# Optimization experiments

Measured on AMD Instinct MI355X. Metric: run time of the kernel, lower is better.

The kernel has to match this reference:

```python
import jax, jax.numpy as jnp
import numpy as np

N_QUBITS = 10
N_LAYERS = 4
BATCH = 16384
IN_FEAT = 256
HIDDEN = 128


def _ry(theta):
    # RY(theta) = [[cos(t/2), -sin(t/2)], [sin(t/2), cos(t/2)]]; theta: (B, n) -> (B, n, 2, 2)
    c = jnp.cos(theta / 2)
    s = jnp.sin(theta / 2)
    row0 = jnp.stack([c, -s], axis=-1)
    row1 = jnp.stack([s, c], axis=-1)
    return jnp.stack([row0, row1], axis=-2).astype(jnp.complex64)


def _rot(phi, theta, omega):
    # PennyLane Rot = RZ(omega) RY(theta) RZ(phi)
    c = jnp.cos(theta / 2)
    s = jnp.sin(theta / 2)
    ep = jnp.exp(-0.5j * (phi + omega))  # e^{-i(phi+omega)/2}
    em = jnp.exp(-0.5j * (phi - omega))  # e^{-i(phi-omega)/2}
    m00 = ep * c
    m01 = -jnp.conj(em) * s
    m10 = em * s
    m11 = jnp.conj(ep) * c
    return jnp.stack([jnp.stack([m00, m01]), jnp.stack([m10, m11])]).astype(jnp.complex64)


def _apply_1q(state, gate, w, n):
    # state: (B, 2**n); gate: (2,2) shared or (B,2,2) per-sample; wire w (wire 0 = MSB)
    B = state.shape[0]
    L, R = 2 ** w, 2 ** (n - w - 1)
    s = state.reshape(B, L, 2, R)
    if gate.ndim == 3:
        s = jnp.einsum('xab,xlbr->xlar', gate, s)
    else:
        s = jnp.einsum('ab,xlbr->xlar', gate, s)
    return s.reshape(B, -1)


def _cnot_perm(n, c, t):
    # CNOT is a basis permutation: flip target bit where control bit is 1 (static numpy)
    idx = np.arange(2 ** n)
    flip = idx ^ (1 << (n - 1 - t))
    ctrl = (idx >> (n - 1 - c)) & 1
    return np.where(ctrl == 1, flip, idx)


def _z_signs(n):
    # (n, 2**n) of +/-1: sign of PauliZ on each wire for each basis state
    idx = np.arange(2 ** n)
    bits = (idx[None, :] >> (n - 1 - np.arange(n)[:, None])) & 1
    return (1.0 - 2.0 * bits).astype(np.float32)


def _circuit(angles, qw):
    # angles: (B, n) embedding angles; qw: (L, n, 3) StronglyEntanglingLayers weights
    B, n = angles.shape
    L = qw.shape[0]
    state = jnp.zeros((B, 2 ** n), jnp.complex64).at[:, 0].set(1.0)
    ry = _ry(angles)  # (B, n, 2, 2) per-sample AngleEmbedding RY gates
    for w in range(n):
        state = _apply_1q(state, ry[:, w], w, n)
    for l in range(L):
        for w in range(n):
            state = _apply_1q(state, _rot(qw[l, w, 0], qw[l, w, 1], qw[l, w, 2]), w, n)
        r = (l % (n - 1)) + 1  # default StronglyEntanglingLayers ranges
        for i in range(n):
            state = state[:, _cnot_perm(n, i, (i + r) % n)]
    probs = jnp.abs(state) ** 2  # (B, 2**n)
    return probs @ jnp.asarray(_z_signs(n)).T  # (B, n) expval PauliZ per wire


def setup_inputs() -> dict:
    key = jax.random.key(0)
    ks = jax.random.split(key, 10)
    d = {
        'x': jax.random.normal(ks[0], (BATCH, IN_FEAT), jnp.float32),
        'W1': jax.random.normal(ks[1], (HIDDEN, IN_FEAT), jnp.float32) / np.sqrt(IN_FEAT),
        'b1': jnp.zeros((HIDDEN,), jnp.float32),
        'W2': jax.random.normal(ks[2], (N_QUBITS, HIDDEN), jnp.float32) / np.sqrt(HIDDEN),
        'b2': jnp.zeros((N_QUBITS,), jnp.float32),
        'q_weights': jax.random.normal(ks[3], (N_LAYERS, N_QUBITS, 3), jnp.float32) * 0.1,
        'W3': jax.random.normal(ks[4], (HIDDEN, N_QUBITS), jnp.float32) / np.sqrt(N_QUBITS),
        'b3': jnp.zeros((HIDDEN,), jnp.float32),
        'W4': jax.random.normal(ks[5], (1, HIDDEN), jnp.float32) / np.sqrt(HIDDEN),
        'b4': jnp.zeros((1,), jnp.float32),
    }
    return d


def reference(x, W1, b1, W2, b2, q_weights, W3, b3, W4, b4):
    # Encoder (dropout is identity in eval mode)
    h = jax.nn.relu(x @ W1.T + b1)
    angles = jnp.tanh(h @ W2.T + b2)  # (B, n_qubits)
    # Batched quantum state-vector simulation
    q = _circuit(angles, q_weights).astype(jnp.float32)  # (B, n_qubits)
    # Decoder
    d = jax.nn.relu(q @ W3.T + b3)
    return d @ W4.T + b4  # (B, 1)
```

## Files before the change

kernel.cpp:

```cpp
#include <hip/hip_runtime.h>
#include <math.h>

#define BATCH 16384
#define INFEAT 256
#define HID 128
#define NQ 10
#define NL 4
#define GSTRIDE 48

typedef float v2f __attribute__((ext_vector_type(2)));

template<int M>
__device__ __forceinline__ float lxor(float x) {
    if constexpr (M == 0) {
        return x;
    } else if constexpr (M < 4) {
        constexpr int ctrl = (0 ^ M) | ((1 ^ M) << 2) | ((2 ^ M) << 4) | ((3 ^ M) << 6);
        return __int_as_float(__builtin_amdgcn_update_dpp(
            __float_as_int(x), __float_as_int(x), ctrl, 0xF, 0xF, false));
    } else if constexpr (M == 8) {
        return __int_as_float(__builtin_amdgcn_update_dpp(
            __float_as_int(x), __float_as_int(x), 0x128, 0xF, 0xF, false));
    } else if constexpr (M < 32) {
        return __int_as_float(__builtin_amdgcn_ds_swizzle(
            __float_as_int(x), (M << 10) | 0x1F));
    } else {
        return __shfl_xor(x, M, 64);
    }
}

__device__ __forceinline__ float dpp_sum(float v) {
    v += __int_as_float(__builtin_amdgcn_update_dpp(0, __float_as_int(v), 0x111, 0xF, 0xF, true));
    v += __int_as_float(__builtin_amdgcn_update_dpp(0, __float_as_int(v), 0x112, 0xF, 0xF, true));
    v += __int_as_float(__builtin_amdgcn_update_dpp(0, __float_as_int(v), 0x114, 0xF, 0xF, true));
    v += __int_as_float(__builtin_amdgcn_update_dpp(0, __float_as_int(v), 0x118, 0xF, 0xF, true));
    v += __int_as_float(__builtin_amdgcn_update_dpp(0, __float_as_int(v), 0x142, 0xF, 0xF, true));
    v += __int_as_float(__builtin_amdgcn_update_dpp(0, __float_as_int(v), 0x143, 0xF, 0xF, true));
    return __int_as_float(__builtin_amdgcn_readlane(__float_as_int(v), 63));
}

template<int HALF>
__device__ __forceinline__ void swap_pl(float& a, float& b) {
    if constexpr (HALF == 32)
        asm("v_permlane32_swap_b32 %0, %1" : "+v"(a), "+v"(b));
    else
        asm("v_permlane16_swap_b32 %0, %1" : "+v"(a), "+v"(b));
}

__device__ __forceinline__ v2f pks_mul(v2f c, v2f a) {
    v2f d; asm("v_pk_mul_f32 %0, %1, %2" : "=v"(d) : "s"(c), "v"(a)); return d;
}
__device__ __forceinline__ v2f pks_fma(v2f c, v2f a, v2f b) {
    v2f d; asm("v_pk_fma_f32 %0, %1, %2, %3" : "=v"(d) : "s"(c), "v"(a), "v"(b)); return d;
}
__device__ __forceinline__ v2f pkv_mul_c(v2f c, v2f a) {
    v2f d; asm("v_pk_mul_f32 %0, %1, %2 op_sel:[0,0] op_sel_hi:[0,1]"
               : "=v"(d) : "v"(c), "v"(a)); return d;
}
__device__ __forceinline__ v2f pkv_fma_c(v2f c, v2f a, v2f b) {
    v2f d; asm("v_pk_fma_f32 %0, %1, %2, %3 op_sel:[0,0,0] op_sel_hi:[0,1,1]"
               : "=v"(d) : "v"(c), "v"(a), "v"(b)); return d;
}
__device__ __forceinline__ v2f pks_mul_blo(v2f c, v2f a) {
    v2f d; asm("v_pk_mul_f32 %0, %1, %2 op_sel:[0,0] op_sel_hi:[1,0]"
               : "=v"(d) : "s"(c), "v"(a)); return d;
}
__device__ __forceinline__ v2f pks_fma_blo(v2f c, v2f a, v2f b) {
    v2f d; asm("v_pk_fma_f32 %0, %1, %2, %3 op_sel:[0,0,0] op_sel_hi:[1,0,1]"
               : "=v"(d) : "s"(c), "v"(a), "v"(b)); return d;
}
__device__ __forceinline__ v2f pks_fma_bhi(v2f c, v2f a, v2f b) {
    v2f d; asm("v_pk_fma_f32 %0, %1, %2, %3 op_sel:[0,1,0] op_sel_hi:[1,1,1]"
               : "=v"(d) : "s"(c), "v"(a), "v"(b)); return d;
}

__device__ __forceinline__ float getv(const v2f (&A)[8], int e) {
    return (e & 1) ? A[e >> 1].y : A[e >> 1].x;
}
__device__ __forceinline__ void setv(v2f (&A)[8], int e, float v) {
    if (e & 1) A[e >> 1].y = v; else A[e >> 1].x = v;
}

template<int KM>
__device__ __forceinline__ void reg_gate_asm(const float* __restrict__ g,
                                             v2f (&AR)[8], v2f (&AI)[8]) {
    const v2f* __restrict__ gp = (const v2f*)g;
    const v2f c00r = gp[6],  c00i = gp[7],  c00in = gp[8];
    const v2f c01r = gp[9],  c01i = gp[10], c01in = gp[11];
    const v2f c10r = gp[12], c10i = gp[13], c10in = gp[14];
    const v2f c11r = gp[15], c11i = gp[16], c11in = gp[17];
#pragma unroll
    for (int k0 = 0; k0 < 8; ++k0) {
        if (k0 & KM) continue;
        const int k1 = k0 | KM;
        v2f A0 = AR[k0], I0 = AI[k0], A1 = AR[k1], I1 = AI[k1];
        v2f t = pks_mul(c00r, A0); t = pks_fma(c00in, I0, t);
        t = pks_fma(c01r, A1, t);  AR[k0] = pks_fma(c01in, I1, t);
        v2f u = pks_mul(c00r, I0); u = pks_fma(c00i, A0, u);
        u = pks_fma(c01r, I1, u);  AI[k0] = pks_fma(c01i, A1, u);
        v2f t2 = pks_mul(c10r, A0); t2 = pks_fma(c10in, I0, t2);
        t2 = pks_fma(c11r, A1, t2); AR[k1] = pks_fma(c11in, I1, t2);
        v2f u2 = pks_mul(c10r, I0); u2 = pks_fma(c10i, A0, u2);
        u2 = pks_fma(c11r, I1, u2); AI[k1] = pks_fma(c11i, A1, u2);
    }
}

__device__ __forceinline__ void reg_gate_q3_asm(const float* __restrict__ g,
                                                v2f (&AR)[8], v2f (&AI)[8]) {
    const v2f* __restrict__ gp = (const v2f*)g;
    const v2f P0 = gp[18], P1 = gp[19], P1n = gp[20];
    const v2f P2 = gp[21], P3 = gp[22], P3n = gp[23];
#pragma unroll
    for (int k = 0; k < 8; ++k) {
        v2f t = pks_mul_blo(P0, AR[k]);
        t = pks_fma_blo(P1n, AI[k], t);
        t = pks_fma_bhi(P2, AR[k], t);
        v2f nR = pks_fma_bhi(P3n, AI[k], t);
        v2f u = pks_mul_blo(P0, AI[k]);
        u = pks_fma_blo(P1, AR[k], u);
        u = pks_fma_bhi(P2, AI[k], u);
        v2f nI = pks_fma_bhi(P3, AR[k], u);
        AR[k] = nR; AI[k] = nI;
    }
}

template<int LB>
__device__ __forceinline__ void lane_gate_asm(const float* __restrict__ g, int lane,
                                              v2f (&AR)[8], v2f (&AI)[8]) {
    const bool side = (lane >> LB) & 1;
    v2f Cmr, Cmi, Cmin, Cpr, Cpi, Cpin;
    Cmr.x  = side ? g[6]  : g[0];
    Cmi.x  = side ? g[7]  : g[1];
    Cmin.x = side ? g[11] : g[8];
    Cpr.x  = side ? g[4]  : g[2];
    Cpi.x  = side ? g[5]  : g[3];
    Cpin.x = side ? g[10] : g[9];
#pragma unroll
    for (int k = 0; k < 8; ++k) {
        v2f PR, PI;
        PR.x = lxor<(1 << LB)>(AR[k].x); PR.y = lxor<(1 << LB)>(AR[k].y);
        PI.x = lxor<(1 << LB)>(AI[k].x); PI.y = lxor<(1 << LB)>(AI[k].y);
        v2f t = pkv_mul_c(Cmr, AR[k]); t = pkv_fma_c(Cmin, AI[k], t);
        t = pkv_fma_c(Cpr, PR, t);     v2f NR = pkv_fma_c(Cpin, PI, t);
        v2f u = pkv_mul_c(Cmr, AI[k]); u = pkv_fma_c(Cmi, AR[k], u);
        u = pkv_fma_c(Cpr, PI, u);     v2f NI = pkv_fma_c(Cpi, PR, u);
        AR[k] = NR; AI[k] = NI;
    }
}

template<int HALF>
__device__ __forceinline__ void lane_gate_pl_asm(const float* __restrict__ g,
                                                 v2f (&AR)[8], v2f (&AI)[8]) {
    const v2f* __restrict__ gp = (const v2f*)g;
    const v2f c00r = gp[6],  c00i = gp[7],  c00in = gp[8];
    const v2f c01r = gp[9],  c01i = gp[10], c01in = gp[11];
    const v2f c10r = gp[12], c10i = gp[13], c10in = gp[14];
    const v2f c11r = gp[15], c11i = gp[16], c11in = gp[17];
#pragma unroll
    for (int k0 = 0; k0 < 8; k0 += 2) {
        const int k1 = k0 + 1;
        float Xr0 = AR[k0].x, Xr1 = AR[k0].y, Yr0 = AR[k1].x, Yr1 = AR[k1].y;
        float Xi0 = AI[k0].x, Xi1 = AI[k0].y, Yi0 = AI[k1].x, Yi1 = AI[k1].y;
        swap_pl<HALF>(Xr0, Yr0); swap_pl<HALF>(Xr1, Yr1);
        swap_pl<HALF>(Xi0, Yi0); swap_pl<HALF>(Xi1, Yi1);
        v2f Xr; Xr.x = Xr0; Xr.y = Xr1;  v2f Yr; Yr.x = Yr0; Yr.y = Yr1;
        v2f Xi; Xi.x = Xi0; Xi.y = Xi1;  v2f Yi; Yi.x = Yi0; Yi.y = Yi1;
        v2f t = pks_mul(c00r, Xr); t = pks_fma(c00in, Xi, t);
        t = pks_fma(c01r, Yr, t);  v2f Pr = pks_fma(c01in, Yi, t);
        v2f u = pks_mul(c00r, Xi); u = pks_fma(c00i, Xr, u);
        u = pks_fma(c01r, Yi, u);  v2f Pi = pks_fma(c01i, Yr, u);
        v2f t2 = pks_mul(c10r, Xr); t2 = pks_fma(c10in, Xi, t2);
        t2 = pks_fma(c11r, Yr, t2); v2f Qr = pks_fma(c11in, Yi, t2);
        v2f u2 = pks_mul(c10r, Xi); u2 = pks_fma(c10i, Xr, u2);
        u2 = pks_fma(c11r, Yi, u2); v2f Qi = pks_fma(c11i, Yr, u2);
        float pr0 = Pr.x, pr1 = Pr.y, qr0 = Qr.x, qr1 = Qr.y;
        float pi0 = Pi.x, pi1 = Pi.y, qi0 = Qi.x, qi1 = Qi.y;
        swap_pl<HALF>(pr0, qr0); swap_pl<HALF>(pr1, qr1);
        swap_pl<HALF>(pi0, qi0); swap_pl<HALF>(pi1, qi1);
        AR[k0].x = pr0; AR[k0].y = pr1; AR[k1].x = qr0; AR[k1].y = qr1;
        AI[k0].x = pi0; AI[k0].y = pi1; AI[k1].x = qi0; AI[k1].y = qi1;
    }
}

constexpr int rr_src(int rs, int e) {
    int s = e;
    for (int i = 3 - rs; i >= 0; --i) s ^= ((s >> (3 - i)) & 1) << (3 - i - rs);
    return s;
}
constexpr int rl_mask(int rs, int e) {
    int m = 0;
    for (int i = (4 - rs < 0 ? 0 : 4 - rs); i <= 3; ++i)
        if ((e >> (3 - i)) & 1) m |= 1 << (9 - i - rs);
    return m;
}

template<int L>
__device__ __forceinline__ void do_gates(const float* __restrict__ gt, int lane,
                                         v2f (&AR)[8], v2f (&AI)[8]) {
    const float* __restrict__ gb = gt + L * NQ * GSTRIDE;
    reg_gate_asm<4>(gb + 0 * GSTRIDE, AR, AI);
    reg_gate_asm<2>(gb + 1 * GSTRIDE, AR, AI);
    reg_gate_asm<1>(gb + 2 * GSTRIDE, AR, AI);
    reg_gate_q3_asm(gb + 3 * GSTRIDE, AR, AI);
    lane_gate_pl_asm<32>(gb + 4 * GSTRIDE, AR, AI);
    lane_gate_pl_asm<16>(gb + 5 * GSTRIDE, AR, AI);
    lane_gate_asm<3>(gb + 6 * GSTRIDE, lane, AR, AI);
    lane_gate_asm<2>(gb + 7 * GSTRIDE, lane, AR, AI);
    lane_gate_asm<1>(gb + 8 * GSTRIDE, lane, AR, AI);
    lane_gate_asm<0>(gb + 9 * GSTRIDE, lane, AR, AI);
}

template<int L>
__device__ __forceinline__ void do_move(int lane, v2f (&AR)[8], v2f (&AI)[8]) {
    constexpr int rs = L + 1;
    int y = lane;
#pragma unroll
    for (int i = 9 - rs; i >= 4; --i)
        y ^= ((y >> (9 - i)) & 1) << (9 - i - rs);
    const int base = y << 2;
    {
        float nr[16], ni[16];
#pragma unroll
        for (int e = 0; e < 16; ++e) {
            const int src = rr_src(rs, e);
            const int am  = rl_mask(rs, e) << 2;
            nr[e] = __int_as_float(__builtin_amdgcn_ds_bpermute(base ^ am, __float_as_int(getv(AR, src))));
            ni[e] = __int_as_float(__builtin_amdgcn_ds_bpermute(base ^ am, __float_as_int(getv(AI, src))));
        }
#pragma unroll
        for (int k = 0; k < 8; ++k) {
            AR[k].x = nr[2 * k]; AR[k].y = nr[2 * k + 1];
            AI[k].x = ni[2 * k]; AI[k].y = ni[2 * k + 1];
        }
    }
#pragma unroll
    for (int i = 10 - rs; i <= 9; ++i) {
        const bool p = (lane >> (9 - i)) & 1;
        const int tm = 1 << (13 - i - rs);
#pragma unroll
        for (int e = 0; e < 16; ++e) {
            if (!(e & tm)) {
                const int e1 = e | tm;
                float v0r = getv(AR, e), v1r = getv(AR, e1);
                setv(AR, e, p ? v1r : v0r); setv(AR, e1, p ? v0r : v1r);
                float v0i = getv(AI, e), v1i = getv(AI, e1);
                setv(AI, e, p ? v1i : v0i); setv(AI, e1, p ? v0i : v1i);
            }
        }
    }
}

__device__ __forceinline__ float ftanh(float s) {
    float e = __expf(2.f * s);
    return 1.f - 2.f / (e + 1.f);
}

__global__ void prep_kernel(const float* __restrict__ qw, const float* __restrict__ W1,
                            float* __restrict__ gtab, float* __restrict__ w1q) {
    int tid = blockIdx.x * 256 + threadIdx.x;
    if (tid < 128 * 64) {
        int k2 = tid >> 6, l = tid & 63;
        float4 q;
        q.x = W1[(size_t)(2 * l)     * INFEAT + 2 * k2];
        q.y = W1[(size_t)(2 * l + 1) * INFEAT + 2 * k2];
        q.z = W1[(size_t)(2 * l)     * INFEAT + 2 * k2 + 1];
        q.w = W1[(size_t)(2 * l + 1) * INFEAT + 2 * k2 + 1];
        ((float4*)w1q)[tid] = q;
    }
    if (blockIdx.x == 0 && threadIdx.x < NL * NQ) {
        int t = threadIdx.x;
        float phi = qw[t * 3 + 0], th = qw[t * 3 + 1], om = qw[t * 3 + 2];
        float c = __cosf(th * 0.5f), s = __sinf(th * 0.5f);
        float a = 0.5f * (phi + om), b = 0.5f * (phi - om);
        float ca = __cosf(a), sa = __sinf(a);
        float cb = __cosf(b), sb = __sinf(b);
        float m00r = ca * c,  m00i = -sa * c;
        float m01r = -cb * s, m01i = -sb * s;
        float m10r = cb * s,  m10i = -sb * s;
        float m11r = ca * c,  m11i = sa * c;
        float* g = gtab + t * GSTRIDE;
        g[0] = m00r; g[1] = m00i; g[2] = m01r; g[3] = m01i;
        g[4] = m10r; g[5] = m10i; g[6] = m11r; g[7] = m11i;
        g[8] = -m00i; g[9] = -m01i; g[10] = -m10i; g[11] = -m11i;
        g[12] = g[13] = m00r;  g[14] = g[15] = m00i;  g[16] = g[17] = -m00i;
        g[18] = g[19] = m01r;  g[20] = g[21] = m01i;  g[22] = g[23] = -m01i;
        g[24] = g[25] = m10r;  g[26] = g[27] = m10i;  g[28] = g[29] = -m10i;
        g[30] = g[31] = m11r;  g[32] = g[33] = m11i;  g[34] = g[35] = -m11i;
        g[36] = m00r;  g[37] = m10r;
        g[38] = m00i;  g[39] = m10i;
        g[40] = -m00i; g[41] = -m10i;
        g[42] = m01r;  g[43] = m11r;
        g[44] = m01i;  g[45] = m11i;
        g[46] = -m01i; g[47] = -m11i;
    }
}

__global__ __launch_bounds__(256, 4) void fused_kernel(
    const float* __restrict__ x, const float* __restrict__ w1q,
    const float* __restrict__ b1, const float* __restrict__ W2,
    const float* __restrict__ b2, const float* __restrict__ gtab,
    const float* __restrict__ W3, const float* __restrict__ b3,
    const float* __restrict__ W4, const float* __restrict__ b4,
    float* __restrict__ out)
{
    __shared__ float w3s[HID * 11];
    __shared__ float b3s[HID], w4s[HID];
    __shared__ float b4s;
    __shared__ v2f hpart[4][4][64];

    const int t = threadIdx.x;
    for (int f = t; f < HID * NQ; f += 256) {
        int c = f / NQ, k = f - c * NQ;
        w3s[c * 11 + k] = W3[f];
    }
    if (t < HID) { b3s[t] = b3[t]; w4s[t] = W4[t]; }
    if (t == 0) b4s = b4[0];

    const int lane = t & 63;
    const int wid = t >> 6;
    const int row0 = blockIdx.x * 4;
    const int ukw = __builtin_amdgcn_readfirstlane(wid);

    v2f acc[4];
#pragma unroll
    for (int r = 0; r < 4; ++r) acc[r] = (v2f)(0.f);
    const float4* __restrict__ xr0 = (const float4*)(x + (size_t)(row0 + 0) * INFEAT + ukw * 64);
    const float4* __restrict__ xr1 = (const float4*)(x + (size_t)(row0 + 1) * INFEAT + ukw * 64);
    const float4* __restrict__ xr2 = (const float4*)(x + (size_t)(row0 + 2) * INFEAT + ukw * 64);
    const float4* __restrict__ xr3 = (const float4*)(x + (size_t)(row0 + 3) * INFEAT + ukw * 64);
    const float4* __restrict__ w1p = (const float4*)w1q + (size_t)ukw * 32 * 64 + lane;
#pragma unroll 4
    for (int kk4 = 0; kk4 < 16; ++kk4) {
        float4 x0 = xr0[kk4], x1 = xr1[kk4], x2 = xr2[kk4], x3 = xr3[kk4];
        float xk[4][4] = {{x0.x, x0.y, x0.z, x0.w}, {x1.x, x1.y, x1.z, x1.w},
                          {x2.x, x2.y, x2.z, x2.w}, {x3.x, x3.y, x3.z, x3.w}};
        float4 q0 = w1p[(2 * kk4 + 0) * 64];
        float4 q1 = w1p[(2 * kk4 + 1) * 64];
        v2f w0; w0.x = q0.x; w0.y = q0.y;
        v2f w1; w1.x = q0.z; w1.y = q0.w;
        v2f w2; w2.x = q1.x; w2.y = q1.y;
        v2f w3; w3.x = q1.z; w3.y = q1.w;
#pragma unroll
        for (int r = 0; r < 4; ++r) {
            v2f xb;
            xb.x = xk[r][0]; xb.y = xk[r][0];
            acc[r] = __builtin_elementwise_fma(xb, w0, acc[r]);
            xb.x = xk[r][1]; xb.y = xk[r][1];
            acc[r] = __builtin_elementwise_fma(xb, w1, acc[r]);
            xb.x = xk[r][2]; xb.y = xk[r][2];
            acc[r] = __builtin_elementwise_fma(xb, w2, acc[r]);
            xb.x = xk[r][3]; xb.y = xk[r][3];
            acc[r] = __builtin_elementwise_fma(xb, w3, acc[r]);
        }
    }
#pragma unroll
    for (int r = 0; r < 4; ++r) hpart[wid][r][lane] = acc[r];
    __syncthreads();

    v2f hs = hpart[0][wid][lane];
    hs += hpart[1][wid][lane];
    hs += hpart[2][wid][lane];
    hs += hpart[3][wid][lane];
    float2 b1v = ((const float2*)b1)[lane];
    float h0 = fmaxf(hs.x + b1v.x, 0.f);
    float h1 = fmaxf(hs.y + b1v.y, 0.f);

    const int row = row0 + wid;

    float cth[NQ], sth[NQ];
#pragma unroll
    for (int w = 0; w < NQ; ++w) {
        float2 w2v = ((const float2*)(W2 + (size_t)w * HID))[lane];
        float aw = dpp_sum(fmaf(h0, w2v.x, h1 * w2v.y)) + b2[w];
        float th = ftanh(aw) * 0.5f;
        cth[w] = __cosf(th); sth[w] = __sinf(th);
    }

    float Lr, Li;
    {
        const float* __restrict__ g = gtab + 4 * GSTRIDE;
        bool bw = (lane >> 5) & 1;
        float g0 = bw ? g[4] : g[0], g1 = bw ? g[5] : g[1];
        float g2 = bw ? g[6] : g[2], g3 = bw ? g[7] : g[3];
        Lr = fmaf(g0, cth[4], g2 * sth[4]);
        Li = fmaf(g1, cth[4], g3 * sth[4]);
    }
#pragma unroll
    for (int w = 5; w < 10; ++w) {
        const float* __restrict__ g = gtab + w * GSTRIDE;
        bool bw = (lane >> (9 - w)) & 1;
        float g0 = bw ? g[4] : g[0], g1 = bw ? g[5] : g[1];
        float g2 = bw ? g[6] : g[2], g3 = bw ? g[7] : g[3];
        float fr = fmaf(g0, cth[w], g2 * sth[w]);
        float fi = fmaf(g1, cth[w], g3 * sth[w]);
        float nr = Lr * fr - Li * fi;
        float ni = Lr * fi + Li * fr;
        Lr = nr; Li = ni;
    }
    float q01r[4], q01i[4], q23r[4], q23i[4];
    {
        const float* __restrict__ ga = gtab + 0 * GSTRIDE;
        const float* __restrict__ gb = gtab + 1 * GSTRIDE;
        float a0r = fmaf(ga[0], cth[0], ga[2] * sth[0]);
        float a0i = fmaf(ga[1], cth[0], ga[3] * sth[0]);
        float b0r = fmaf(ga[4], cth[0], ga[6] * sth[0]);
        float b0i = fmaf(ga[5], cth[0], ga[7] * sth[0]);
        float a1r = fmaf(gb[0], cth[1], gb[2] * sth[1]);
        float a1i = fmaf(gb[1], cth[1], gb[3] * sth[1]);
        float b1r = fmaf(gb[4], cth[1], gb[6] * sth[1]);
        float b1i = fmaf(gb[5], cth[1], gb[7] * sth[1]);
#pragma unroll
        for (int j = 0; j < 4; ++j) {
            float f0r = (j & 2) ? b0r : a0r, f0i = (j & 2) ? b0i : a0i;
            float f1r = (j & 1) ? b1r : a1r, f1i = (j & 1) ? b1i : a1i;
            q01r[j] = f0r * f1r - f0i * f1i;
            q01i[j] = f0r * f1i + f0i * f1r;
        }
    }
    {
        const float* __restrict__ ga = gtab + 2 * GSTRIDE;
        const float* __restrict__ gb = gtab + 3 * GSTRIDE;
        float a2r = fmaf(ga[0], cth[2], ga[2] * sth[2]);
        float a2i = fmaf(ga[1], cth[2], ga[3] * sth[2]);
        float b2r = fmaf(ga[4], cth[2], ga[6] * sth[2]);
        float b2i = fmaf(ga[5], cth[2], ga[7] * sth[2]);
        float a3r = fmaf(gb[0], cth[3], gb[2] * sth[3]);
        float a3i = fmaf(gb[1], cth[3], gb[3] * sth[3]);
        float b3r = fmaf(gb[4], cth[3], gb[6] * sth[3]);
        float b3i = fmaf(gb[5], cth[3], gb[7] * sth[3]);
#pragma unroll
        for (int j = 0; j < 4; ++j) {
            float f2r = (j & 2) ? b2r : a2r, f2i = (j & 2) ? b2i : a2i;
            float f3r = (j & 1) ? b3r : a3r, f3i = (j & 1) ? b3i : a3i;
            q23r[j] = f2r * f3r - f2i * f3i;
            q23i[j] = f2r * f3i + f2i * f3r;
        }
    }
    v2f AR[8], AI[8];
#pragma unroll
    for (int e = 0; e < 16; ++e) {
        const int jh = e >> 2, jl = e & 3;
        float tr = q01r[jh] * q23r[jl] - q01i[jh] * q23i[jl];
        float ti = q01r[jh] * q23i[jl] + q01i[jh] * q23r[jl];
        float ar = tr * Lr - ti * Li;
        float ai = tr * Li + ti * Lr;
        setv(AR, e, ar); setv(AI, e, ai);
    }

    do_move<0>(lane, AR, AI);
    do_gates<1>(gtab, lane, AR, AI);
    do_move<1>(lane, AR, AI);
    do_gates<2>(gtab, lane, AR, AI);
    do_move<2>(lane, AR, AI);
    do_gates<3>(gtab, lane, AR, AI);
    do_move<3>(lane, AR, AI);

    v2f Pk[8];
#pragma unroll
    for (int k = 0; k < 8; ++k) Pk[k] = AR[k] * AR[k] + AI[k] * AI[k];
    v2f S = Pk[0] + Pk[1] + Pk[2] + Pk[3] + Pk[4] + Pk[5] + Pk[6] + Pk[7];
    float ptot = S.x + S.y;
    v2f Sq0 = Pk[4] + Pk[5] + Pk[6] + Pk[7];
    v2f Sq1 = Pk[2] + Pk[3] + Pk[6] + Pk[7];
    v2f Sq2 = Pk[1] + Pk[3] + Pk[5] + Pk[7];
    float es0 = dpp_sum(ptot - 2.f * (Sq0.x + Sq0.y));
    float es1 = dpp_sum(ptot - 2.f * (Sq1.x + Sq1.y));
    float es2 = dpp_sum(ptot - 2.f * (Sq2.x + Sq2.y));
    float es3 = dpp_sum(ptot - 2.f * S.y);
    float Wv = ptot;
    {
        float p;
        p = lxor<1>(Wv);  Wv = (lane & 1)  ? p - Wv : Wv + p;
        p = lxor<2>(Wv);  Wv = (lane & 2)  ? p - Wv : Wv + p;
        p = lxor<4>(Wv);  Wv = (lane & 4)  ? p - Wv : Wv + p;
        p = lxor<8>(Wv);  Wv = (lane & 8)  ? p - Wv : Wv + p;
        p = lxor<16>(Wv); Wv = (lane & 16) ? p - Wv : Wv + p;
        p = lxor<32>(Wv); Wv = (lane & 32) ? p - Wv : Wv + p;
    }
    const int wvi = __float_as_int(Wv);
    float es[NQ];
    es[0] = es0; es[1] = es1; es[2] = es2; es[3] = es3;
    es[4] = __int_as_float(__builtin_amdgcn_readlane(wvi, 32));
    es[5] = __int_as_float(__builtin_amdgcn_readlane(wvi, 16));
    es[6] = __int_as_float(__builtin_amdgcn_readlane(wvi, 8));
    es[7] = __int_as_float(__builtin_amdgcn_readlane(wvi, 4));
    es[8] = __int_as_float(__builtin_amdgcn_readlane(wvi, 2));
    es[9] = __int_as_float(__builtin_amdgcn_readlane(wvi, 1));

    float accv = 0.f;
#pragma unroll
    for (int j = 0; j < 2; ++j) {
        int c = lane + 64 * j;
        float d = b3s[c];
#pragma unroll
        for (int k = 0; k < NQ; ++k) d = fmaf(w3s[c * 11 + k], es[k], d);
        d = fmaxf(d, 0.f);
        accv = fmaf(d, w4s[c], accv);
    }
    accv = dpp_sum(accv);
    if (lane == 0) out[row] = accv + b4s;
}

extern "C" void kernel_launch(void* const* d_in, const int* in_sizes, int n_in,
                              void* d_out, int out_size, void* d_ws, size_t ws_size,
                              hipStream_t stream) {
    const float* x  = (const float*)d_in[0];
    const float* W1 = (const float*)d_in[1];
    const float* b1 = (const float*)d_in[2];
    const float* W2 = (const float*)d_in[3];
    const float* b2 = (const float*)d_in[4];
    const float* qw = (const float*)d_in[5];
    const float* W3 = (const float*)d_in[6];
    const float* b3 = (const float*)d_in[7];
    const float* W4 = (const float*)d_in[8];
    const float* b4 = (const float*)d_in[9];
    float* gtab = (float*)d_ws;
    float* w1q  = (float*)d_ws + 2048;
    float* out  = (float*)d_out;

    prep_kernel<<<(128 * 64 + 255) / 256, 256, 0, stream>>>(qw, W1, gtab, w1q);
    fused_kernel<<<BATCH / 4, 256, 0, stream>>>(x, w1q, b1, W2, b2, gtab, W3, b3, W4, b4, out);
}
```

Measured before the change: 214.9 us.

## Factor Rot gates into real RY plus merged diagonal phase tables

Each PennyLane Rot gate is split as RZ·RY·RZ. All RZ phases between consecutive RY layers, including those carried through the CNOT permutation, are folded into one precomputed per-basis-state diagonal phase table. The 10 general complex gates per layer become real RY rotations with far fewer packed FMAs, plus one complex diagonal multiply per layer loaded from a workspace table. The cost is extra global or L2 loads of the phase table (8 float4 per lane per layer) and a heavier prep kernel computing the phases in double precision.

```diff
diff --git a/kernel.cpp b/kernel.cpp
--- a/kernel.cpp
+++ b/kernel.cpp
@@ -53,6 +53,10 @@
 __device__ __forceinline__ v2f pks_fma(v2f c, v2f a, v2f b) {
     v2f d; asm("v_pk_fma_f32 %0, %1, %2, %3" : "=v"(d) : "s"(c), "v"(a), "v"(b)); return d;
 }
+__device__ __forceinline__ v2f pks_fma_swap(v2f c, v2f a, v2f b) {
+    v2f d; asm("v_pk_fma_f32 %0, %1, %2, %3 op_sel:[0,1,0] op_sel_hi:[1,0,1]"
+               : "=v"(d) : "s"(c), "v"(a), "v"(b)); return d;
+}
 __device__ __forceinline__ v2f pkv_mul_c(v2f c, v2f a) {
     v2f d; asm("v_pk_mul_f32 %0, %1, %2 op_sel:[0,0] op_sel_hi:[0,1]"
                : "=v"(d) : "v"(c), "v"(a)); return d;
@@ -61,18 +65,6 @@
     v2f d; asm("v_pk_fma_f32 %0, %1, %2, %3 op_sel:[0,0,0] op_sel_hi:[0,1,1]"
                : "=v"(d) : "v"(c), "v"(a), "v"(b)); return d;
 }
-__device__ __forceinline__ v2f pks_mul_blo(v2f c, v2f a) {
-    v2f d; asm("v_pk_mul_f32 %0, %1, %2 op_sel:[0,0] op_sel_hi:[1,0]"
-               : "=v"(d) : "s"(c), "v"(a)); return d;
-}
-__device__ __forceinline__ v2f pks_fma_blo(v2f c, v2f a, v2f b) {
-    v2f d; asm("v_pk_fma_f32 %0, %1, %2, %3 op_sel:[0,0,0] op_sel_hi:[1,0,1]"
-               : "=v"(d) : "s"(c), "v"(a), "v"(b)); return d;
-}
-__device__ __forceinline__ v2f pks_fma_bhi(v2f c, v2f a, v2f b) {
-    v2f d; asm("v_pk_fma_f32 %0, %1, %2, %3 op_sel:[0,1,0] op_sel_hi:[1,1,1]"
-               : "=v"(d) : "s"(c), "v"(a), "v"(b)); return d;
-}
 
 __device__ __forceinline__ float getv(const v2f (&A)[8], int e) {
     return (e & 1) ? A[e >> 1].y : A[e >> 1].x;
@@ -81,81 +73,40 @@
     if (e & 1) A[e >> 1].y = v; else A[e >> 1].x = v;
 }
 
+
 template<int KM>
-__device__ __forceinline__ void reg_gate_asm(const float* __restrict__ g,
-                                             v2f (&AR)[8], v2f (&AI)[8]) {
+__device__ __forceinline__ void reg_ry(const float* __restrict__ g,
+                                       v2f (&AR)[8], v2f (&AI)[8]) {
     const v2f* __restrict__ gp = (const v2f*)g;
-    const v2f c00r = gp[6],  c00i = gp[7],  c00in = gp[8];
-    const v2f c01r = gp[9],  c01i = gp[10], c01in = gp[11];
-    const v2f c10r = gp[12], c10i = gp[13], c10in = gp[14];
-    const v2f c11r = gp[15], c11i = gp[16], c11in = gp[17];
+    const v2f C = gp[6], S = gp[7], Sn = gp[8];
 #pragma unroll
     for (int k0 = 0; k0 < 8; ++k0) {
         if (k0 & KM) continue;
         const int k1 = k0 | KM;
-        v2f A0 = AR[k0], I0 = AI[k0], A1 = AR[k1], I1 = AI[k1];
-        v2f t = pks_mul(c00r, A0); t = pks_fma(c00in, I0, t);
-        t = pks_fma(c01r, A1, t);  AR[k0] = pks_fma(c01in, I1, t);
-        v2f u = pks_mul(c00r, I0); u = pks_fma(c00i, A0, u);
-        u = pks_fma(c01r, I1, u);  AI[k0] = pks_fma(c01i, A1, u);
-        v2f t2 = pks_mul(c10r, A0); t2 = pks_fma(c10in, I0, t2);
-        t2 = pks_fma(c11r, A1, t2); AR[k1] = pks_fma(c11in, I1, t2);
-        v2f u2 = pks_mul(c10r, I0); u2 = pks_fma(c10i, A0, u2);
-        u2 = pks_fma(c11r, I1, u2); AI[k1] = pks_fma(c11i, A1, u2);
-    }
-}
-
-__device__ __forceinline__ void reg_gate_q3_asm(const float* __restrict__ g,
-                                                v2f (&AR)[8], v2f (&AI)[8]) {
+        v2f A0 = AR[k0], A1 = AR[k1], I0 = AI[k0], I1 = AI[k1];
+        AR[k0] = pks_fma(Sn, A1, pks_mul(C, A0));
+        AI[k0] = pks_fma(Sn, I1, pks_mul(C, I0));
+        AR[k1] = pks_fma(C, A1, pks_mul(S, A0));
+        AI[k1] = pks_fma(C, I1, pks_mul(S, I0));
+    }
+}
+
+__device__ __forceinline__ void q3_ry(const float* __restrict__ g,
+                                      v2f (&AR)[8], v2f (&AI)[8]) {
     const v2f* __restrict__ gp = (const v2f*)g;
-    const v2f P0 = gp[18], P1 = gp[19], P1n = gp[20];
-    const v2f P2 = gp[21], P3 = gp[22], P3n = gp[23];
+    const v2f C = gp[9], Ssw = gp[10];
 #pragma unroll
     for (int k = 0; k < 8; ++k) {
-        v2f t = pks_mul_blo(P0, AR[k]);
-        t = pks_fma_blo(P1n, AI[k], t);
-        t = pks_fma_bhi(P2, AR[k], t);
-        v2f nR = pks_fma_bhi(P3n, AI[k], t);
-        v2f u = pks_mul_blo(P0, AI[k]);
-        u = pks_fma_blo(P1, AR[k], u);
-        u = pks_fma_bhi(P2, AI[k], u);
-        v2f nI = pks_fma_bhi(P3, AR[k], u);
-        AR[k] = nR; AI[k] = nI;
-    }
-}
-
-template<int LB>
-__device__ __forceinline__ void lane_gate_asm(const float* __restrict__ g, int lane,
-                                              v2f (&AR)[8], v2f (&AI)[8]) {
-    const bool side = (lane >> LB) & 1;
-    v2f Cmr, Cmi, Cmin, Cpr, Cpi, Cpin;
-    Cmr.x  = side ? g[6]  : g[0];
-    Cmi.x  = side ? g[7]  : g[1];
-    Cmin.x = side ? g[11] : g[8];
-    Cpr.x  = side ? g[4]  : g[2];
-    Cpi.x  = side ? g[5]  : g[3];
-    Cpin.x = side ? g[10] : g[9];
-#pragma unroll
-    for (int k = 0; k < 8; ++k) {
-        v2f PR, PI;
-        PR.x = lxor<(1 << LB)>(AR[k].x); PR.y = lxor<(1 << LB)>(AR[k].y);
-        PI.x = lxor<(1 << LB)>(AI[k].x); PI.y = lxor<(1 << LB)>(AI[k].y);
-        v2f t = pkv_mul_c(Cmr, AR[k]); t = pkv_fma_c(Cmin, AI[k], t);
-        t = pkv_fma_c(Cpr, PR, t);     v2f NR = pkv_fma_c(Cpin, PI, t);
-        v2f u = pkv_mul_c(Cmr, AI[k]); u = pkv_fma_c(Cmi, AR[k], u);
-        u = pkv_fma_c(Cpr, PI, u);     v2f NI = pkv_fma_c(Cpi, PR, u);
-        AR[k] = NR; AI[k] = NI;
+        AR[k] = pks_fma_swap(Ssw, AR[k], pks_mul(C, AR[k]));
+        AI[k] = pks_fma_swap(Ssw, AI[k], pks_mul(C, AI[k]));
     }
 }
 
 template<int HALF>
-__device__ __forceinline__ void lane_gate_pl_asm(const float* __restrict__ g,
-                                                 v2f (&AR)[8], v2f (&AI)[8]) {
+__device__ __forceinline__ void pl_ry(const float* __restrict__ g,
+                                      v2f (&AR)[8], v2f (&AI)[8]) {
     const v2f* __restrict__ gp = (const v2f*)g;
-    const v2f c00r = gp[6],  c00i = gp[7],  c00in = gp[8];
-    const v2f c01r = gp[9],  c01i = gp[10], c01in = gp[11];
-    const v2f c10r = gp[12], c10i = gp[13], c10in = gp[14];
-    const v2f c11r = gp[15], c11i = gp[16], c11in = gp[17];
+    const v2f C = gp[6], S = gp[7], Sn = gp[8];
 #pragma unroll
     for (int k0 = 0; k0 < 8; k0 += 2) {
         const int k1 = k0 + 1;
@@ -165,14 +116,10 @@
         swap_pl<HALF>(Xi0, Yi0); swap_pl<HALF>(Xi1, Yi1);
         v2f Xr; Xr.x = Xr0; Xr.y = Xr1;  v2f Yr; Yr.x = Yr0; Yr.y = Yr1;
         v2f Xi; Xi.x = Xi0; Xi.y = Xi1;  v2f Yi; Yi.x = Yi0; Yi.y = Yi1;
-        v2f t = pks_mul(c00r, Xr); t = pks_fma(c00in, Xi, t);
-        t = pks_fma(c01r, Yr, t);  v2f Pr = pks_fma(c01in, Yi, t);
-        v2f u = pks_mul(c00r, Xi); u = pks_fma(c00i, Xr, u);
-        u = pks_fma(c01r, Yi, u);  v2f Pi = pks_fma(c01i, Yr, u);
-        v2f t2 = pks_mul(c10r, Xr); t2 = pks_fma(c10in, Xi, t2);
-        t2 = pks_fma(c11r, Yr, t2); v2f Qr = pks_fma(c11in, Yi, t2);
-        v2f u2 = pks_mul(c10r, Xi); u2 = pks_fma(c10i, Xr, u2);
-        u2 = pks_fma(c11r, Yi, u2); v2f Qi = pks_fma(c11i, Yr, u2);
+        v2f Pr = pks_fma(Sn, Yr, pks_mul(C, Xr));
+        v2f Pi = pks_fma(Sn, Yi, pks_mul(C, Xi));
+        v2f Qr = pks_fma(C, Yr, pks_mul(S, Xr));
+        v2f Qi = pks_fma(C, Yi, pks_mul(S, Xi));
         float pr0 = Pr.x, pr1 = Pr.y, qr0 = Qr.x, qr1 = Qr.y;
         float pi0 = Pi.x, pi1 = Pi.y, qi0 = Qi.x, qi1 = Qi.y;
         swap_pl<HALF>(pr0, qr0); swap_pl<HALF>(pr1, qr1);
@@ -182,6 +129,38 @@
     }
 }
 
+template<int LB>
+__device__ __forceinline__ void lane_ry(const float* __restrict__ g, int lane,
+                                        v2f (&AR)[8], v2f (&AI)[8]) {
+    const bool side = (lane >> LB) & 1;
+    v2f Cm, Cp;
+    Cm.x = g[8];
+    Cp.x = side ? g[10] : g[9];
+#pragma unroll
+    for (int k = 0; k < 8; ++k) {
+        v2f PR, PI;
+        PR.x = lxor<(1 << LB)>(AR[k].x); PR.y = lxor<(1 << LB)>(AR[k].y);
+        PI.x = lxor<(1 << LB)>(AI[k].x); PI.y = lxor<(1 << LB)>(AI[k].y);
+        AR[k] = pkv_fma_c(Cp, PR, pkv_mul_c(Cm, AR[k]));
+        AI[k] = pkv_fma_c(Cp, PI, pkv_mul_c(Cm, AI[k]));
+    }
+}
+
+__device__ __forceinline__ void apply_diag(const float* __restrict__ dt, int lane,
+                                           v2f (&AR)[8], v2f (&AI)[8]) {
+    const float4* __restrict__ d4 = (const float4*)dt;
+#pragma unroll
+    for (int k = 0; k < 8; ++k) {
+        float4 q = d4[k * 64 + lane];
+        v2f CR; CR.x = q.x; CR.y = q.y;
+        v2f CI; CI.x = q.z; CI.y = q.w;
+        v2f ar = AR[k], ai = AI[k];
+        v2f nR = __builtin_elementwise_fma(CI, -ai, CR * ar);
+        v2f nI = __builtin_elementwise_fma(CI, ar, CR * ai);
+        AR[k] = nR; AI[k] = nI;
+    }
+}
+
 constexpr int rr_src(int rs, int e) {
     int s = e;
     for (int i = 3 - rs; i >= 0; --i) s ^= ((s >> (3 - i)) & 1) << (3 - i - rs);
@@ -195,19 +174,19 @@
 }
 
 template<int L>
-__device__ __forceinline__ void do_gates(const float* __restrict__ gt, int lane,
-                                         v2f (&AR)[8], v2f (&AI)[8]) {
+__device__ __forceinline__ void do_gates_ry(const float* __restrict__ gt, int lane,
+                                            v2f (&AR)[8], v2f (&AI)[8]) {
     const float* __restrict__ gb = gt + L * NQ * GSTRIDE;
-    reg_gate_asm<4>(gb + 0 * GSTRIDE, AR, AI);
-    reg_gate_asm<2>(gb + 1 * GSTRIDE, AR, AI);
-    reg_gate_asm<1>(gb + 2 * GSTRIDE, AR, AI);
-    reg_gate_q3_asm(gb + 3 * GSTRIDE, AR, AI);
-    lane_gate_pl_asm<32>(gb + 4 * GSTRIDE, AR, AI);
-    lane_gate_pl_asm<16>(gb + 5 * GSTRIDE, AR, AI);
-    lane_gate_asm<3>(gb + 6 * GSTRIDE, lane, AR, AI);
-    lane_gate_asm<2>(gb + 7 * GSTRIDE, lane, AR, AI);
-    lane_gate_asm<1>(gb + 8 * GSTRIDE, lane, AR, AI);
-    lane_gate_asm<0>(gb + 9 * GSTRIDE, lane, AR, AI);
+    reg_ry<4>(gb + 0 * GSTRIDE, AR, AI);
+    reg_ry<2>(gb + 1 * GSTRIDE, AR, AI);
+    reg_ry<1>(gb + 2 * GSTRIDE, AR, AI);
+    q3_ry(gb + 3 * GSTRIDE, AR, AI);
+    pl_ry<32>(gb + 4 * GSTRIDE, AR, AI);
+    pl_ry<16>(gb + 5 * GSTRIDE, AR, AI);
+    lane_ry<3>(gb + 6 * GSTRIDE, lane, AR, AI);
+    lane_ry<2>(gb + 7 * GSTRIDE, lane, AR, AI);
+    lane_ry<1>(gb + 8 * GSTRIDE, lane, AR, AI);
+    lane_ry<0>(gb + 9 * GSTRIDE, lane, AR, AI);
 }
 
 template<int L>
@@ -256,7 +235,8 @@
 }
 
 __global__ void prep_kernel(const float* __restrict__ qw, const float* __restrict__ W1,
-                            float* __restrict__ gtab, float* __restrict__ w1q) {
+                            float* __restrict__ gtab, float* __restrict__ w1q,
+                            float* __restrict__ dtab) {
     int tid = blockIdx.x * 256 + threadIdx.x;
     if (tid < 128 * 64) {
         int k2 = tid >> 6, l = tid & 63;
@@ -281,17 +261,44 @@
         float* g = gtab + t * GSTRIDE;
         g[0] = m00r; g[1] = m00i; g[2] = m01r; g[3] = m01i;
         g[4] = m10r; g[5] = m10i; g[6] = m11r; g[7] = m11i;
-        g[8] = -m00i; g[9] = -m01i; g[10] = -m10i; g[11] = -m11i;
-        g[12] = g[13] = m00r;  g[14] = g[15] = m00i;  g[16] = g[17] = -m00i;
-        g[18] = g[19] = m01r;  g[20] = g[21] = m01i;  g[22] = g[23] = -m01i;
-        g[24] = g[25] = m10r;  g[26] = g[27] = m10i;  g[28] = g[29] = -m10i;
-        g[30] = g[31] = m11r;  g[32] = g[33] = m11i;  g[34] = g[35] = -m11i;
-        g[36] = m00r;  g[37] = m10r;
-        g[38] = m00i;  g[39] = m10i;
-        g[40] = -m00i; g[41] = -m10i;
-        g[42] = m01r;  g[43] = m11r;
-        g[44] = m01i;  g[45] = m11i;
-        g[46] = -m01i; g[47] = -m11i;
+        g[8] = c;  g[9] = -s;  g[10] = s;  g[11] = 0.f;
+        g[12] = c;  g[13] = c;
+        g[14] = s;  g[15] = s;
+        g[16] = -s; g[17] = -s;
+        g[18] = c;  g[19] = c;
+        g[20] = -s; g[21] = s;
+    }
+    if (tid < 3 * 8 * 64) {
+        const int ld = tid >> 9;
+        const int k = (tid >> 6) & 7;
+        const int lane = tid & 63;
+        float cr[2], ci[2];
+#pragma unroll
+        for (int h = 0; h < 2; ++h) {
+            const int n = ((2 * k + h) << 6) | lane;
+            double a = 0.0;
+            for (int w = 0; w < NQ; ++w) {
+                const double bit = (double)((n >> (9 - w)) & 1) - 0.5;
+                a += (double)qw[(ld + 1) * NQ * 3 + w * 3 + 0] * bit;
+            }
+            if (ld >= 1) {
+                const int r = ld + 1;
+                int m = n;
+                for (int i = 9; i >= 0; --i) {
+                    const int tq = (i + r) % 10;
+                    m ^= ((m >> (9 - i)) & 1) << (9 - tq);
+                }
+                for (int w = 0; w < NQ; ++w) {
+                    const double bit = (double)((m >> (9 - w)) & 1) - 0.5;
+                    a += (double)qw[ld * NQ * 3 + w * 3 + 2] * bit;
+                }
+            }
+            cr[h] = (float)cos(a);
+            ci[h] = (float)sin(a);
+        }
+        float4 o;
+        o.x = cr[0]; o.y = cr[1]; o.z = ci[0]; o.w = ci[1];
+        ((float4*)dtab)[tid] = o;
     }
 }
 
@@ -299,6 +306,7 @@
     const float* __restrict__ x, const float* __restrict__ w1q,
     const float* __restrict__ b1, const float* __restrict__ W2,
     const float* __restrict__ b2, const float* __restrict__ gtab,
+    const float* __restrict__ dtab,
     const float* __restrict__ W3, const float* __restrict__ b3,
     const float* __restrict__ W4, const float* __restrict__ b4,
     float* __restrict__ out)
@@ -448,11 +456,14 @@
     }
 
     do_move<0>(lane, AR, AI);
-    do_gates<1>(gtab, lane, AR, AI);
+    apply_diag(dtab + 0 * 2048, lane, AR, AI);
+    do_gates_ry<1>(gtab, lane, AR, AI);
     do_move<1>(lane, AR, AI);
-    do_gates<2>(gtab, lane, AR, AI);
+    apply_diag(dtab + 1 * 2048, lane, AR, AI);
+    do_gates_ry<2>(gtab, lane, AR, AI);
     do_move<2>(lane, AR, AI);
-    do_gates<3>(gtab, lane, AR, AI);
+    apply_diag(dtab + 2 * 2048, lane, AR, AI);
+    do_gates_ry<3>(gtab, lane, AR, AI);
     do_move<3>(lane, AR, AI);
 
     v2f Pk[8];
@@ -516,8 +527,9 @@
     const float* b4 = (const float*)d_in[9];
     float* gtab = (float*)d_ws;
     float* w1q  = (float*)d_ws + 2048;
+    float* dtab = (float*)d_ws + 2048 + 32768;
     float* out  = (float*)d_out;
 
-    prep_kernel<<<(128 * 64 + 255) / 256, 256, 0, stream>>>(qw, W1, gtab, w1q);
-    fused_kernel<<<BATCH / 4, 256, 0, stream>>>(x, w1q, b1, W2, b2, gtab, W3, b3, W4, b4, out);
-}
+    prep_kernel<<<(128 * 64 + 255) / 256, 256, 0, stream>>>(qw, W1, gtab, w1q, dtab);
+    fused_kernel<<<BATCH / 4, 256, 0, stream>>>(x, w1q, b1, W2, b2, gtab, dtab, W3, b3, W4, b4, out);
+}
```

New measurement: 187.2 us. -12.9%, faster.
